# Kernel tuning notes

Hardware: AMD Instinct MI355X
Metric: run time of the kernel (lower is better)

## Reference

```python
import jax, jax.numpy as jnp
import numpy as np

K = 16          # nodes_num
BN_EPS = 1e-5


def _bn_conv_relu(x, w, gamma, beta, mean, var):
    # 1x1 conv on [N,K,C] node features == matmul, then eval-mode BN + ReLU
    y = jnp.einsum('nkc,oc->nko', x, w)                      # [N,K,256]
    y = (y - mean) * jax.lax.rsqrt(var + BN_EPS) * gamma + beta
    return jax.nn.relu(y)


def _lnorm(r, c):
    # Symmetric-normalized affinity from node pixel coordinates.
    # A_ij = 1/(1+||p_i-p_j||), self-loops A_ii=1, Lnorm = D^-1/2 A D^-1/2
    p = jnp.stack([r, c], axis=-1).astype(jnp.float32)        # [N,K,2]
    diff = p[:, :, None, :] - p[:, None, :, :]
    dist = jnp.sqrt(jnp.sum(diff * diff, axis=-1))            # [N,K,K]
    A = 1.0 / (1.0 + dist)
    dinv = jax.lax.rsqrt(jnp.sum(A, axis=-1))                 # [N,K]
    return A * dinv[:, :, None] * dinv[:, None, :]


def setup_inputs() -> dict:
    key = jax.random.key(0)
    ks = jax.random.split(key, 12)
    N, C, W, H = 128, 1024, 14, 14
    O = 256
    inp = {
        'fpam_output': jax.random.normal(ks[0], (N, C, W, H), jnp.float32),
        'resnet_output': jax.random.normal(ks[1], (N, 2048), jnp.float32),
        'w_max': jax.random.normal(ks[2], (O, C), jnp.float32) * 0.02,
        'g_max': 1.0 + 0.1 * jax.random.normal(ks[3], (O,), jnp.float32),
        'b_max': 0.1 * jax.random.normal(ks[4], (O,), jnp.float32),
        'm_max': 0.1 * jax.random.normal(ks[5], (O,), jnp.float32),
        'v_max': jax.random.uniform(ks[6], (O,), jnp.float32, 0.5, 1.5),
        'w_med': jax.random.normal(ks[7], (O, C), jnp.float32) * 0.02,
        'g_med': 1.0 + 0.1 * jax.random.normal(ks[8], (O,), jnp.float32),
        'b_med': 0.1 * jax.random.normal(ks[9], (O,), jnp.float32),
        'm_med': 0.1 * jax.random.normal(ks[10], (O,), jnp.float32),
        'v_med': jax.random.uniform(ks[11], (O,), jnp.float32, 0.5, 1.5),
    }
    return inp


def reference(fpam_output, resnet_output, w_max, g_max, b_max, m_max, v_max,
              w_med, g_med, b_med, m_med, v_med):
    N, C, W, H = fpam_output.shape
    HW = W * H
    # channel-sum saliency, sort descending
    fre = jnp.sum(fpam_output, axis=1).reshape(N, HW)         # [N,HW]
    idx = jnp.argsort(-fre, axis=1)
    maxK = idx[:, :K]
    mstart = HW // 2 - K // 2 - 1
    medK = idx[:, mstart:mstart + K]
    scene = jnp.concatenate([maxK, medK], axis=1)             # [N,2K]
    rows = scene // H
    cols = scene % H
    # batched gather replacing the per-pixel python loop
    flat = fpam_output.reshape(N, C, HW)
    nodes = jnp.take_along_axis(flat, scene[:, None, :], axis=2)  # [N,C,2K]
    nodes = jnp.transpose(nodes, (0, 2, 1))                   # [N,2K,C]
    x_max = _bn_conv_relu(nodes[:, :K], w_max, g_max, b_max, m_max, v_max)
    x_med = _bn_conv_relu(nodes[:, K:], w_med, g_med, b_med, m_med, v_med)
    Ltop = _lnorm(rows[:, :K], cols[:, :K])
    Lmed = _lnorm(rows[:, K:], cols[:, K:])
    max_graph = jnp.einsum('nij,njc->nic', Ltop, x_max).reshape(N, -1)
    med_graph = jnp.einsum('nij,njc->nic', Lmed, x_med).reshape(N, -1)
    return (max_graph, med_graph, rows, cols)
```

## Files before the change

### kernel.cpp

```cpp
#include <hip/hip_runtime.h>

#define NB 128
#define CC 1024
#define HWP 196
#define HH 14
#define OO 256

typedef unsigned short ushort_t;
typedef __attribute__((ext_vector_type(8))) short short8;
typedef __attribute__((ext_vector_type(4))) float float4v;

__device__ __forceinline__ ushort_t f2bf(float v) {
  union { float f; unsigned int u; } c; c.f = v;
  unsigned int u = c.u;
  unsigned int r = (u + 0x7FFFu + ((u >> 16) & 1u)) >> 16;
  return (ushort_t)r;
}

__global__ __launch_bounds__(256) void k_reduce(const float* __restrict__ x,
                                                float* __restrict__ partial) {
  int n = blockIdx.x, cg = blockIdx.y;
  int p = threadIdx.x;
  if (p >= HWP) return;
  const float* base = x + ((size_t)n * CC + (size_t)cg * 128) * HWP + p;
  float s = 0.f;
  #pragma unroll 8
  for (int c = 0; c < 128; ++c) s += base[(size_t)c * HWP];
  partial[(n * 8 + cg) * HWP + p] = s;
}

__global__ __launch_bounds__(256) void k_select(const float* __restrict__ partial,
                                                int* __restrict__ scene,
                                                float* __restrict__ out) {
  int n = blockIdx.x, t = threadIdx.x;
  __shared__ float fre[HWP];
  __shared__ int sc[32];
  if (t < HWP) {
    float s = 0.f;
    #pragma unroll
    for (int g = 0; g < 8; ++g) s += partial[(n * 8 + g) * HWP + t];
    fre[t] = s;
  }
  __syncthreads();
  if (t < HWP) {
    float v = fre[t];
    int rank = 0;
    for (int q = 0; q < HWP; ++q) {
      float u = fre[q];
      rank += ((u > v) || (u == v && q < t)) ? 1 : 0;
    }
    if (rank < 16) sc[rank] = t;
    else if (rank >= 89 && rank < 105) sc[rank - 73] = t;
  }
  __syncthreads();
  if (t < 32) {
    int p = sc[t];
    scene[n * 32 + t] = p;
    out[2 * NB * 4096 + n * 32 + t] = (float)(p / HH);
    out[2 * NB * 4096 + NB * 32 + n * 32 + t] = (float)(p % HH);
  }
}

__global__ __launch_bounds__(256) void k_convw(const float* __restrict__ wmax,
                                               const float* __restrict__ wmed,
                                               ushort_t* __restrict__ wb) {
  int idx = blockIdx.x * 256 + threadIdx.x;
  int z = idx >> 18;
  int r = idx & (OO * CC - 1);
  const float* w = z ? wmed : wmax;
  wb[idx] = f2bf(w[r]);
}

__global__ __launch_bounds__(256) void k_main(
    const float* __restrict__ x, const ushort_t* __restrict__ wb,
    const float* __restrict__ g_max, const float* __restrict__ b_max,
    const float* __restrict__ m_max, const float* __restrict__ v_max,
    const float* __restrict__ g_med, const float* __restrict__ b_med,
    const float* __restrict__ m_med, const float* __restrict__ v_med,
    const int* __restrict__ scene, float* __restrict__ out) {
  constexpr int AP = 1032;
  __shared__ ushort_t A_sh[16 * AP];
  __shared__ float Lsh[16][17];
  __shared__ float dinv[16];
  __shared__ int s_sh[16];
  __shared__ float y_sh[16][257];

  const int n = blockIdx.x;
  const int z = blockIdx.y;
  const int t = threadIdx.x;

  if (t < 16) s_sh[t] = scene[n * 32 + z * 16 + t];
  __syncthreads();

  {
    const int j = t & 15;
    const int kg = t >> 4;
    const int sj = s_sh[j];
    const float* xb = x + (size_t)n * (CC * HWP) + sj;
    ushort_t* arow = &A_sh[j * AP];
    #pragma unroll 8
    for (int u = 0; u < 64; ++u) {
      int k = kg * 64 + u;
      arow[k] = f2bf(xb[(size_t)k * HWP]);
    }
  }
  {
    const int i = t >> 4, j = t & 15;
    int pi = s_sh[i], pj = s_sh[j];
    float dr = (float)(pi / HH - pj / HH);
    float dc = (float)(pi % HH - pj % HH);
    Lsh[i][j] = 1.0f / (1.0f + sqrtf(dr * dr + dc * dc));
  }
  __syncthreads();
  if (t < 16) {
    float s = 0.f;
    #pragma unroll
    for (int j = 0; j < 16; ++j) s += Lsh[t][j];
    dinv[t] = rsqrtf(s);
  }

  const int w = t >> 6;
  const int l = t & 63;
  const int m = l & 15;
  const int quad = l >> 4;

  const ushort_t* Arow = &A_sh[m * AP + quad * 8];
  const ushort_t* B0 = wb + (size_t)z * (OO * CC) + (size_t)(w * 64 + m) * CC + quad * 8;

  float4v acc0 = {0.f, 0.f, 0.f, 0.f};
  float4v acc1 = acc0, acc2 = acc0, acc3 = acc0;

  __syncthreads();

  #pragma unroll 2
  for (int k0 = 0; k0 < CC; k0 += 32) {
    short8 a  = *reinterpret_cast<const short8*>(Arow + k0);
    short8 b0 = *reinterpret_cast<const short8*>(B0 + k0);
    short8 b1 = *reinterpret_cast<const short8*>(B0 + 16 * CC + k0);
    short8 b2 = *reinterpret_cast<const short8*>(B0 + 32 * CC + k0);
    short8 b3 = *reinterpret_cast<const short8*>(B0 + 48 * CC + k0);
    acc0 = __builtin_amdgcn_mfma_f32_16x16x32_bf16(a, b0, acc0, 0, 0, 0);
    acc1 = __builtin_amdgcn_mfma_f32_16x16x32_bf16(a, b1, acc1, 0, 0, 0);
    acc2 = __builtin_amdgcn_mfma_f32_16x16x32_bf16(a, b2, acc2, 0, 0, 0);
    acc3 = __builtin_amdgcn_mfma_f32_16x16x32_bf16(a, b3, acc3, 0, 0, 0);
  }

  const float* gp = z ? g_med : g_max;
  const float* bp = z ? b_med : b_max;
  const float* mp = z ? m_med : m_max;
  const float* vp = z ? v_med : v_max;

  #pragma unroll
  for (int tt = 0; tt < 4; ++tt) {
    float4v av = (tt == 0) ? acc0 : (tt == 1) ? acc1 : (tt == 2) ? acc2 : acc3;
    int o = w * 64 + tt * 16 + m;
    float sc = gp[o] * rsqrtf(vp[o] + 1e-5f);
    float sh = bp[o] - mp[o] * sc;
    #pragma unroll
    for (int r = 0; r < 4; ++r) {
      int j = quad * 4 + r;
      float y = av[r] * sc + sh;
      y = fmaxf(y, 0.f);
      y_sh[j][o] = y * dinv[j];
    }
  }
  __syncthreads();

  float yp[16];
  #pragma unroll
  for (int j = 0; j < 16; ++j) yp[j] = y_sh[j][t];
  float* ob = out + (size_t)z * (NB * 4096) + (size_t)n * 4096 + t;
  #pragma unroll
  for (int i = 0; i < 16; ++i) {
    float s = 0.f;
    #pragma unroll
    for (int j = 0; j < 16; ++j) s = fmaf(Lsh[i][j], yp[j], s);
    ob[(size_t)i * OO] = s * dinv[i];
  }
}

extern "C" void kernel_launch(void* const* d_in, const int* in_sizes, int n_in,
                              void* d_out, int out_size, void* d_ws, size_t ws_size,
                              hipStream_t stream) {
  const float* x     = (const float*)d_in[0];
  const float* w_max = (const float*)d_in[2];
  const float* g_max = (const float*)d_in[3];
  const float* b_max = (const float*)d_in[4];
  const float* m_max = (const float*)d_in[5];
  const float* v_max = (const float*)d_in[6];
  const float* w_med = (const float*)d_in[7];
  const float* g_med = (const float*)d_in[8];
  const float* b_med = (const float*)d_in[9];
  const float* m_med = (const float*)d_in[10];
  const float* v_med = (const float*)d_in[11];
  float* out = (float*)d_out;

  float* ws_f = (float*)d_ws;
  float* partial  = ws_f;
  int* scene      = (int*)(ws_f + 200704);
  ushort_t* wb    = (ushort_t*)(ws_f + 204800);

  k_reduce<<<dim3(NB, 8), 256, 0, stream>>>(x, partial);
  k_select<<<dim3(NB), 256, 0, stream>>>(partial, scene, out);
  k_convw<<<dim3((2 * OO * CC) / 256), 256, 0, stream>>>(w_max, w_med, wb);
  k_main<<<dim3(NB, 2), 256, 0, stream>>>(x, wb, g_max, b_max, m_max, v_max,
                                          g_med, b_med, m_med, v_med, scene, out);
}
```

Measured before the change: 212.4 us.

## Gather selected node features in a separate coalesced kernel before matmul

Adds a k_gather kernel that streams 8-channel slabs of the input into shared memory with float4 loads, picks the 32 selected pixels per sample, converts them to bf16 and writes a compact [N,32,C] node buffer. k_main then fills its A tile with 16-byte loads from that buffer instead of doing strided scalar gathers from the full input. This targets the uncoalesced, low-parallelism gather inside k_main, but it re-reads the whole input tensor (about 100 MB) and adds one more launch. The MFMA loop unroll factor is also raised from 2 to 4.

```diff
diff --git a/kernel.cpp b/kernel.cpp
--- a/kernel.cpp
+++ b/kernel.cpp
@@ -61,6 +61,24 @@
   }
 }
 
+__global__ __launch_bounds__(256) void k_gather(const float* __restrict__ x,
+                                                const int* __restrict__ scene,
+                                                ushort_t* __restrict__ nodes) {
+  int n = blockIdx.x, cs = blockIdx.y, t = threadIdx.x;
+  __shared__ alignas(16) float buf[8 * HWP];
+  __shared__ int s_sh[32];
+  if (t < 32) s_sh[t] = scene[n * 32 + t];
+  const int jj = t >> 3, cc = t & 7;
+  for (int c0 = 0; c0 < 128; c0 += 8) {
+    const float4* src = (const float4*)(x + ((size_t)n * CC + (size_t)cs * 128 + c0) * HWP);
+    __syncthreads();
+    for (int i = t; i < (8 * HWP) / 4; i += 256) ((float4*)buf)[i] = src[i];
+    __syncthreads();
+    float v = buf[cc * HWP + s_sh[jj]];
+    nodes[((size_t)n * 32 + jj) * CC + (size_t)cs * 128 + c0 + cc] = f2bf(v);
+  }
+}
+
 __global__ __launch_bounds__(256) void k_convw(const float* __restrict__ wmax,
                                                const float* __restrict__ wmed,
                                                ushort_t* __restrict__ wb) {
@@ -72,7 +90,7 @@
 }
 
 __global__ __launch_bounds__(256) void k_main(
-    const float* __restrict__ x, const ushort_t* __restrict__ wb,
+    const ushort_t* __restrict__ nodes, const ushort_t* __restrict__ wb,
     const float* __restrict__ g_max, const float* __restrict__ b_max,
     const float* __restrict__ m_max, const float* __restrict__ v_max,
     const float* __restrict__ g_med, const float* __restrict__ b_med,
@@ -90,20 +108,18 @@
   const int t = threadIdx.x;
 
   if (t < 16) s_sh[t] = scene[n * 32 + z * 16 + t];
-  __syncthreads();
 
   {
-    const int j = t & 15;
-    const int kg = t >> 4;
-    const int sj = s_sh[j];
-    const float* xb = x + (size_t)n * (CC * HWP) + sj;
-    ushort_t* arow = &A_sh[j * AP];
-    #pragma unroll 8
-    for (int u = 0; u < 64; ++u) {
-      int k = kg * 64 + u;
-      arow[k] = f2bf(xb[(size_t)k * HWP]);
+    const ushort_t* src = nodes + ((size_t)n * 32 + (size_t)z * 16) * CC;
+    #pragma unroll
+    for (int i = t; i < 2048; i += 256) {
+      int j = i >> 7, c8 = i & 127;
+      *reinterpret_cast<short8*>(&A_sh[j * AP + c8 * 8]) =
+          *reinterpret_cast<const short8*>(&src[j * CC + c8 * 8]);
     }
   }
+  __syncthreads();
+
   {
     const int i = t >> 4, j = t & 15;
     int pi = s_sh[i], pj = s_sh[j];
@@ -132,7 +148,7 @@
 
   __syncthreads();
 
-  #pragma unroll 2
+  #pragma unroll 4
   for (int k0 = 0; k0 < CC; k0 += 32) {
     short8 a  = *reinterpret_cast<const short8*>(Arow + k0);
     short8 b0 = *reinterpret_cast<const short8*>(B0 + k0);
@@ -199,10 +215,12 @@
   float* partial  = ws_f;
   int* scene      = (int*)(ws_f + 200704);
   ushort_t* wb    = (ushort_t*)(ws_f + 204800);
+  ushort_t* nodes = (ushort_t*)(ws_f + 466944);
 
   k_reduce<<<dim3(NB, 8), 256, 0, stream>>>(x, partial);
   k_select<<<dim3(NB), 256, 0, stream>>>(partial, scene, out);
   k_convw<<<dim3((2 * OO * CC) / 256), 256, 0, stream>>>(w_max, w_med, wb);
-  k_main<<<dim3(NB, 2), 256, 0, stream>>>(x, wb, g_max, b_max, m_max, v_max,
+  k_gather<<<dim3(NB, 8), 256, 0, stream>>>(x, scene, nodes);
+  k_main<<<dim3(NB, 2), 256, 0, stream>>>(nodes, wb, g_max, b_max, m_max, v_max,
                                           g_med, b_med, m_med, v_med, scene, out);
 }
```

New measurement: 222.1 us. 1.05x slower.

## Merge four launches into two: fuse reduce with weight convert, select into main

Applied to the files above, without the earlier changes.

Folds the weight bf16 conversion into the channel-reduction kernel as extra blocks, and moves the top-K ranking selection into the main GEMM kernel. Each main block recomputes the selection for its sample, so the scene buffer round-trip and two launches go away. It also raises the unroll factors on the reduction and MFMA loops. The cost is that the ranking work is done twice per sample, once for each z, which lengthens the main kernel's prologue.

```diff
diff --git a/kernel.cpp b/kernel.cpp
--- a/kernel.cpp
+++ b/kernel.cpp
@@ -17,34 +17,61 @@
   return (ushort_t)r;
 }
 
-__global__ __launch_bounds__(256) void k_reduce(const float* __restrict__ x,
-                                                float* __restrict__ partial) {
-  int n = blockIdx.x, cg = blockIdx.y;
-  int p = threadIdx.x;
+__global__ __launch_bounds__(256) void k_prep(const float* __restrict__ x,
+                                              const float* __restrict__ wmax,
+                                              const float* __restrict__ wmed,
+                                              float* __restrict__ partial,
+                                              ushort_t* __restrict__ wb) {
+  const int b = blockIdx.x, t = threadIdx.x;
+  if (b >= 1024) {
+    int idx = (b - 1024) * 256 + t;
+    int z = idx >> 18;
+    int r = idx & (OO * CC - 1);
+    const float* w = z ? wmed : wmax;
+    wb[idx] = f2bf(w[r]);
+    return;
+  }
+  const int n = b >> 3, cg = b & 7;
+  const int p = t;
   if (p >= HWP) return;
   const float* base = x + ((size_t)n * CC + (size_t)cg * 128) * HWP + p;
   float s = 0.f;
-  #pragma unroll 8
+  #pragma unroll 16
   for (int c = 0; c < 128; ++c) s += base[(size_t)c * HWP];
-  partial[(n * 8 + cg) * HWP + p] = s;
-}
-
-__global__ __launch_bounds__(256) void k_select(const float* __restrict__ partial,
-                                                int* __restrict__ scene,
-                                                float* __restrict__ out) {
-  int n = blockIdx.x, t = threadIdx.x;
+  partial[((size_t)n * 8 + cg) * HWP + p] = s;
+}
+
+__global__ __launch_bounds__(256) void k_main(
+    const float* __restrict__ x, const float* __restrict__ partial,
+    const ushort_t* __restrict__ wb,
+    const float* __restrict__ g_max, const float* __restrict__ b_max,
+    const float* __restrict__ m_max, const float* __restrict__ v_max,
+    const float* __restrict__ g_med, const float* __restrict__ b_med,
+    const float* __restrict__ m_med, const float* __restrict__ v_med,
+    float* __restrict__ out) {
+  constexpr int AP = 1032;
+  __shared__ ushort_t A_sh[16 * AP];
   __shared__ float fre[HWP];
   __shared__ int sc[32];
+  __shared__ float Lsh[16][17];
+  __shared__ float dinv[16];
+  __shared__ float y_sh[16][257];
+
+  const int n = blockIdx.x;
+  const int z = blockIdx.y;
+  const int t = threadIdx.x;
+
   if (t < HWP) {
     float s = 0.f;
     #pragma unroll
-    for (int g = 0; g < 8; ++g) s += partial[(n * 8 + g) * HWP + t];
+    for (int g = 0; g < 8; ++g) s += partial[((size_t)n * 8 + g) * HWP + t];
     fre[t] = s;
   }
   __syncthreads();
   if (t < HWP) {
     float v = fre[t];
     int rank = 0;
+    #pragma unroll 4
     for (int q = 0; q < HWP; ++q) {
       float u = fre[q];
       rank += ((u > v) || (u == v && q < t)) ? 1 : 0;
@@ -53,49 +80,17 @@
     else if (rank >= 89 && rank < 105) sc[rank - 73] = t;
   }
   __syncthreads();
-  if (t < 32) {
+
+  if (z == 0 && t < 32) {
     int p = sc[t];
-    scene[n * 32 + t] = p;
     out[2 * NB * 4096 + n * 32 + t] = (float)(p / HH);
     out[2 * NB * 4096 + NB * 32 + n * 32 + t] = (float)(p % HH);
   }
-}
-
-__global__ __launch_bounds__(256) void k_convw(const float* __restrict__ wmax,
-                                               const float* __restrict__ wmed,
-                                               ushort_t* __restrict__ wb) {
-  int idx = blockIdx.x * 256 + threadIdx.x;
-  int z = idx >> 18;
-  int r = idx & (OO * CC - 1);
-  const float* w = z ? wmed : wmax;
-  wb[idx] = f2bf(w[r]);
-}
-
-__global__ __launch_bounds__(256) void k_main(
-    const float* __restrict__ x, const ushort_t* __restrict__ wb,
-    const float* __restrict__ g_max, const float* __restrict__ b_max,
-    const float* __restrict__ m_max, const float* __restrict__ v_max,
-    const float* __restrict__ g_med, const float* __restrict__ b_med,
-    const float* __restrict__ m_med, const float* __restrict__ v_med,
-    const int* __restrict__ scene, float* __restrict__ out) {
-  constexpr int AP = 1032;
-  __shared__ ushort_t A_sh[16 * AP];
-  __shared__ float Lsh[16][17];
-  __shared__ float dinv[16];
-  __shared__ int s_sh[16];
-  __shared__ float y_sh[16][257];
-
-  const int n = blockIdx.x;
-  const int z = blockIdx.y;
-  const int t = threadIdx.x;
-
-  if (t < 16) s_sh[t] = scene[n * 32 + z * 16 + t];
-  __syncthreads();
 
   {
     const int j = t & 15;
     const int kg = t >> 4;
-    const int sj = s_sh[j];
+    const int sj = sc[z * 16 + j];
     const float* xb = x + (size_t)n * (CC * HWP) + sj;
     ushort_t* arow = &A_sh[j * AP];
     #pragma unroll 8
@@ -106,7 +101,7 @@
   }
   {
     const int i = t >> 4, j = t & 15;
-    int pi = s_sh[i], pj = s_sh[j];
+    int pi = sc[z * 16 + i], pj = sc[z * 16 + j];
     float dr = (float)(pi / HH - pj / HH);
     float dc = (float)(pi % HH - pj % HH);
     Lsh[i][j] = 1.0f / (1.0f + sqrtf(dr * dr + dc * dc));
@@ -132,7 +127,7 @@
 
   __syncthreads();
 
-  #pragma unroll 2
+  #pragma unroll 4
   for (int k0 = 0; k0 < CC; k0 += 32) {
     short8 a  = *reinterpret_cast<const short8*>(Arow + k0);
     short8 b0 = *reinterpret_cast<const short8*>(B0 + k0);
@@ -154,12 +149,12 @@
   for (int tt = 0; tt < 4; ++tt) {
     float4v av = (tt == 0) ? acc0 : (tt == 1) ? acc1 : (tt == 2) ? acc2 : acc3;
     int o = w * 64 + tt * 16 + m;
-    float sc = gp[o] * rsqrtf(vp[o] + 1e-5f);
-    float sh = bp[o] - mp[o] * sc;
+    float scale = gp[o] * rsqrtf(vp[o] + 1e-5f);
+    float shift = bp[o] - mp[o] * scale;
     #pragma unroll
     for (int r = 0; r < 4; ++r) {
       int j = quad * 4 + r;
-      float y = av[r] * sc + sh;
+      float y = av[r] * scale + shift;
       y = fmaxf(y, 0.f);
       y_sh[j][o] = y * dinv[j];
     }
@@ -197,12 +192,10 @@
 
   float* ws_f = (float*)d_ws;
   float* partial  = ws_f;
-  int* scene      = (int*)(ws_f + 200704);
-  ushort_t* wb    = (ushort_t*)(ws_f + 204800);
-
-  k_reduce<<<dim3(NB, 8), 256, 0, stream>>>(x, partial);
-  k_select<<<dim3(NB), 256, 0, stream>>>(partial, scene, out);
-  k_convw<<<dim3((2 * OO * CC) / 256), 256, 0, stream>>>(w_max, w_med, wb);
-  k_main<<<dim3(NB, 2), 256, 0, stream>>>(x, wb, g_max, b_max, m_max, v_max,
-                                          g_med, b_med, m_med, v_med, scene, out);
-}
+  ushort_t* wb    = (ushort_t*)(ws_f + 200704);
+
+  k_prep<<<dim3(1024 + 2048), 256, 0, stream>>>(x, w_max, w_med, partial, wb);
+  k_main<<<dim3(NB, 2), 256, 0, stream>>>(x, partial, wb,
+                                          g_max, b_max, m_max, v_max,
+                                          g_med, b_med, m_med, v_med, out);
+}
```

Result: no change. 211.4 us (-0.5%).
